# Kernel tuning notes

Hardware: AMD Instinct MI355X
Metric: run time of the kernel (lower is better)

Reference implementation:

```python
import jax, jax.numpy as jnp
import numpy as np

IN_C = 128
OUT_C = 128
N = 100000
E = 1600000


def spmm(row, col, w, x, n):
    # out[i] = sum_{e: row[e]==i} w[e] * x[col[e]]  (sparse adjacency matmul)
    return jax.ops.segment_sum(w[:, None] * x[col], row, num_segments=n)


def setup_inputs() -> dict:
    key = jax.random.key(0)
    ks = jax.random.split(key, 10)
    x = jax.random.normal(ks[0], (N, IN_C), dtype=jnp.float32)
    row = jax.random.randint(ks[1], (E,), 0, N, dtype=jnp.int32)
    col = jax.random.randint(ks[2], (E,), 0, N, dtype=jnp.int32)
    edge_weight = jax.random.uniform(ks[3], (E,), dtype=jnp.float32)
    s = 1.0 / np.sqrt(IN_C)
    W0 = jax.random.uniform(ks[4], (IN_C, OUT_C), minval=-s, maxval=s, dtype=jnp.float32)
    b0 = jax.random.uniform(ks[5], (OUT_C,), minval=-s, maxval=s, dtype=jnp.float32)
    W1 = jax.random.uniform(ks[6], (IN_C, OUT_C), minval=-s, maxval=s, dtype=jnp.float32)
    b1 = jax.random.uniform(ks[7], (OUT_C,), minval=-s, maxval=s, dtype=jnp.float32)
    W2 = jax.random.uniform(ks[8], (IN_C, OUT_C), minval=-s, maxval=s, dtype=jnp.float32)
    b2 = jax.random.uniform(ks[9], (OUT_C,), minval=-s, maxval=s, dtype=jnp.float32)
    return {"x": x, "row": row, "col": col, "edge_weight": edge_weight,
            "W0": W0, "b0": b0, "W1": W1, "b1": b1, "W2": W2, "b2": b2}


def reference(x, row, col, edge_weight, W0, b0, W1, b1, W2, b2):
    n = x.shape[0]
    # hop 0: plain linear
    x0 = x @ W0 + b0
    # hop 1: linear then one SpMM propagation
    x1 = spmm(row, col, edge_weight, x @ W1 + b1, n)
    # hop 2: linear then two SpMM propagations
    x2 = spmm(row, col, edge_weight,
              spmm(row, col, edge_weight, x @ W2 + b2, n), n)
    return jnp.concatenate([x0, x1, x2], axis=1)  # [N, 3*OUT_C]
```

## Files before the change

### kernel.cpp

```cpp
#include <hip/hip_runtime.h>

typedef __attribute__((ext_vector_type(8))) short bf16x8;
typedef __attribute__((ext_vector_type(4))) float f32x4;
typedef __attribute__((ext_vector_type(2))) float f32x2;
typedef __attribute__((ext_vector_type(2))) uint u32x2;
typedef __attribute__((ext_vector_type(4))) uint u32x4;

static inline size_t align256(size_t x) { return (x + 255) & ~size_t(255); }

__device__ inline ushort f2bf(float f) {
  uint u = __float_as_uint(f);
  return (ushort)((u + 0x7FFFu + ((u >> 16) & 1u)) >> 16);
}
__device__ inline float bf2f(ushort h) { return __uint_as_float(((uint)h) << 16); }


__device__ inline uint fp8x4_enc(float a0, float a1, float a2, float a3) {
#if __has_builtin(__builtin_amdgcn_cvt_pk_fp8_f32)
  int v = 0;
  v = __builtin_amdgcn_cvt_pk_fp8_f32(a0, a1, v, false);
  v = __builtin_amdgcn_cvt_pk_fp8_f32(a2, a3, v, true);
  return (uint)v;
#else
  float a[4] = {a0, a1, a2, a3};
  uint r = 0;
#pragma unroll
  for (int k = 0; k < 4; ++k) {
    uint u = __float_as_uint(a[k]);
    uint s = (u >> 24) & 0x80u;
    uint au = u & 0x7FFFFFFFu;
    uint b;
    if (au < 0x3C800000u) {
      b = s;
    } else {
      uint rr = au + 0x7FFFFu + ((au >> 20) & 1u);
      uint e = (rr >> 23) - 120u;
      uint m = (rr >> 20) & 7u;
      b = s | (e << 3) | m;
    }
    r |= b << (8 * k);
  }
  return r;
#endif
}

__device__ inline f32x4 fp8x4_dec(uint u) {
  f32x4 r;
#if __has_builtin(__builtin_amdgcn_cvt_pk_f32_fp8)
  auto lo = __builtin_amdgcn_cvt_pk_f32_fp8((int)u, false);
  auto hi = __builtin_amdgcn_cvt_pk_f32_fp8((int)u, true);
  r[0] = lo[0]; r[1] = lo[1]; r[2] = hi[0]; r[3] = hi[1];
#else
#pragma unroll
  for (int k = 0; k < 4; ++k) {
    uint b = (u >> (8 * k)) & 0xFFu;
    uint f = ((b & 0x80u) << 24) | (((b & 0x7Fu) + (120u << 3)) << 20);
    r[k] = (b & 0x7Fu) ? __uint_as_float(f) : 0.f;
  }
#endif
  return r;
}

#define BW_SHIFT 7
#define NBUCK_MAX 1024
#define NCHUNK 256
#define PREP_BLOCKS 96


__global__ __launch_bounds__(512) void build_a_kernel(
    const int* __restrict__ row, int* __restrict__ bcnt,
    int* __restrict__ chunk_hist, int E, int chunk,
    const float* __restrict__ W0, const float* __restrict__ W1,
    const float* __restrict__ W2, ushort* __restrict__ Wt,
    int* __restrict__ done, int* __restrict__ boff, int* __restrict__ gcur,
    int* __restrict__ offp, int n) {
  __shared__ int h[NBUCK_MAX];
  int bid = blockIdx.x;
  int t = threadIdx.x;
  if (bid < NCHUNK) {
    for (int i = t; i < NBUCK_MAX; i += 512) h[i] = 0;
    __syncthreads();
    int c0 = bid * chunk, c1 = min(c0 + chunk, E);
    for (int i = c0 + t; i < c1; i += 512)
      atomicAdd(&h[row[i] >> BW_SHIFT], 1);
    __syncthreads();
    for (int i = t; i < NBUCK_MAX; i += 512) {
      int c = h[i];
      chunk_hist[bid * NBUCK_MAX + i] = c;
      if (c) atomicAdd(&bcnt[i], c);
    }
  } else {
    int i = (bid - NCHUNK) * 512 + t;
    int mat = i >> 14, r = i & 16383;
    int k = r >> 7, c = r & 127;
    const float* W = (mat == 0) ? W0 : (mat == 1) ? W1 : W2;
    Wt[mat * 16384 + c * 128 + k] = f2bf(W[k * 128 + c]);
  }
  __shared__ int ticket;
  __syncthreads();
  if (t == 0) {
    __threadfence();
    ticket = atomicAdd(done, 1);
  }
  __syncthreads();
  if (ticket == (int)gridDim.x - 1) {
    __threadfence();
    int v0 = bcnt[2 * t], v1 = bcnt[2 * t + 1];
    int pair = v0 + v1;
    h[t] = pair;
    __syncthreads();
    for (int o = 1; o < 512; o <<= 1) {
      int a = (t >= o) ? h[t - o] : 0;
      __syncthreads();
      h[t] += a;
      __syncthreads();
    }
    int excl = h[t] - pair;
    boff[2 * t] = excl;          gcur[2 * t] = excl;
    boff[2 * t + 1] = excl + v0; gcur[2 * t + 1] = excl + v0;
    if (t == 511) boff[NBUCK_MAX] = E;
    if (t == 0) offp[n] = E;
  }
}


__global__ __launch_bounds__(512) void bin_scatter(
    const int* __restrict__ row, const int* __restrict__ col,
    const float* __restrict__ w, int* __restrict__ gcur,
    const int* __restrict__ chunk_hist, int2* __restrict__ es_tmp,
    int E, int chunk) {
  __shared__ int lbase[NBUCK_MAX];
  __shared__ int lh[NBUCK_MAX];
  int bid = blockIdx.x;
  int t = threadIdx.x;
  for (int i = t; i < NBUCK_MAX; i += 512) {
    int c = chunk_hist[bid * NBUCK_MAX + i];
    lbase[i] = c ? atomicAdd(&gcur[i], c) : 0;
    lh[i] = 0;
  }
  __syncthreads();
  int c0 = bid * chunk, c1 = min(c0 + chunk, E);
  for (int i = c0 + t; i < c1; i += 512) {
    int r = row[i];
    int b = r >> BW_SHIFT;
    int pos = lbase[b] + atomicAdd(&lh[b], 1);
    es_tmp[pos] = make_int2(((r & 127) << 17) | col[i], __float_as_int(w[i]));
  }
}


__global__ __launch_bounds__(256) void bucket_sort(const int2* __restrict__ es_tmp,
                                                   const int* __restrict__ boff,
                                                   int2* __restrict__ es,
                                                   int* __restrict__ offp, int n) {
  __shared__ int lh[128];
  __shared__ int lex[128];
  int b = blockIdx.x;
  int base = boff[b], cnt = boff[b + 1] - base;
  int t = threadIdx.x;
  if (t < 128) lh[t] = 0;
  __syncthreads();
  for (int i = t; i < cnt; i += 256)
    atomicAdd(&lh[(es_tmp[base + i].x >> 17) & 127], 1);
  __syncthreads();
  if (t < 128) lex[t] = lh[t];
  __syncthreads();
  for (int o = 1; o < 128; o <<= 1) {
    int a = (t >= o && t < 128) ? lex[t - o] : 0;
    __syncthreads();
    if (t < 128) lex[t] += a;
    __syncthreads();
  }
  if (t < 128) {
    int v = lh[t];
    int excl = lex[t] - v;
    int node = (b << BW_SHIFT) + t;
    if (node < n) offp[node] = base + excl;
    lh[t] = excl;
  }
  __syncthreads();
  for (int i = t; i < cnt; i += 256) {
    int2 ed = es_tmp[base + i];
    int nl = (ed.x >> 17) & 127;
    int pos = base + atomicAdd(&lh[nl], 1);
    es[pos] = make_int2(ed.x & 0x1FFFF, ed.y);
  }
}


__global__ __launch_bounds__(256) void gemm3_kernel(
    const float* __restrict__ x, const ushort* __restrict__ Wt,
    const float* __restrict__ b0, const float* __restrict__ b1,
    const float* __restrict__ b2,
    float* __restrict__ out0,
    unsigned char* __restrict__ y12,
    int n) {
  int w = threadIdx.x >> 6;
  int l = threadIdx.x & 63;
  int lr = l & 15;
  int lg = l >> 4;
  int rows0 = blockIdx.x * 256 + w * 64;

  bf16x8 xf[4][4];
#pragma unroll
  for (int rt = 0; rt < 4; ++rt) {
    int row = rows0 + rt * 16 + lr;
    bool ok = row < n;
    const float* base = x + (size_t)row * 128;
#pragma unroll
    for (int kc = 0; kc < 4; ++kc) {
      float4 a = ok ? *(const float4*)(base + kc * 32 + lg * 8) : make_float4(0, 0, 0, 0);
      float4 c = ok ? *(const float4*)(base + kc * 32 + lg * 8 + 4) : make_float4(0, 0, 0, 0);
      bf16x8 f;
      f[0] = (short)f2bf(a.x); f[1] = (short)f2bf(a.y);
      f[2] = (short)f2bf(a.z); f[3] = (short)f2bf(a.w);
      f[4] = (short)f2bf(c.x); f[5] = (short)f2bf(c.y);
      f[6] = (short)f2bf(c.z); f[7] = (short)f2bf(c.w);
      xf[rt][kc] = f;
    }
  }

  for (int mat = 0; mat < 3; ++mat) {
    const ushort* Wm = Wt + mat * 16384;
    const float* bias = (mat == 0) ? b0 : (mat == 1) ? b1 : b2;
#pragma unroll 1
    for (int ct = 0; ct < 8; ++ct) {
      bf16x8 wf[4];
#pragma unroll
      for (int kc = 0; kc < 4; ++kc)
        wf[kc] = *(const bf16x8*)(Wm + (ct * 16 + lr) * 128 + kc * 32 + lg * 8);
      float4 bb = *(const float4*)(bias + ct * 16 + lg * 4);
      f32x4 acc[4];
#pragma unroll
      for (int rt = 0; rt < 4; ++rt) {
        acc[rt][0] = bb.x; acc[rt][1] = bb.y; acc[rt][2] = bb.z; acc[rt][3] = bb.w;
      }
#pragma unroll
      for (int kc = 0; kc < 4; ++kc)
#pragma unroll
        for (int rt = 0; rt < 4; ++rt)
          acc[rt] = __builtin_amdgcn_mfma_f32_16x16x32_bf16(wf[kc], xf[rt][kc], acc[rt], 0, 0, 0);
#pragma unroll
      for (int rt = 0; rt < 4; ++rt) {
        int row = rows0 + rt * 16 + lr;
        if (row >= n) continue;
        int col = ct * 16 + lg * 4;
        if (mat == 0) {
          __builtin_nontemporal_store(acc[rt], (f32x4*)(out0 + (size_t)row * 384 + col));
        } else {
          uint v8 = fp8x4_enc(acc[rt][0], acc[rt][1], acc[rt][2], acc[rt][3]);
          unsigned char* Y = y12 + (size_t)row * 256 + ((mat == 2) ? 128 : 0) + col;
          *(uint*)Y = v8;
        }
      }
    }
  }
}


__global__ __launch_bounds__(256) void spmm_dual_kernel(
    const unsigned char* __restrict__ y12,
    float* __restrict__ o1,
    ushort* __restrict__ z2,
    const int* __restrict__ off, const int2* __restrict__ es, int n) {
  int node = blockIdx.x * 8 + ((threadIdx.x >> 6) << 1) + ((threadIdx.x & 63) >> 5);
  if (node >= n) return;
  int h = threadIdx.x & 31;
  int s = off[node], e = off[node + 1];
  float a0 = 0.f, a1 = 0.f, a2 = 0.f, a3 = 0.f;
  float a4 = 0.f, a5 = 0.f, a6 = 0.f, a7 = 0.f;
  int i = s;
  for (; i + 4 <= e; i += 4) {
    u32x2 u[4];
    float w[4];
#pragma unroll
    for (int j = 0; j < 4; ++j) {
      int2 ed = es[i + j];
      w[j] = __int_as_float(ed.y);
      u[j] = *(const u32x2*)(y12 + (size_t)ed.x * 256 + h * 8);
    }
#pragma unroll
    for (int j = 0; j < 4; ++j) {
      f32x4 p = fp8x4_dec(u[j].x), q = fp8x4_dec(u[j].y);
      a0 += w[j] * p[0]; a1 += w[j] * p[1]; a2 += w[j] * p[2]; a3 += w[j] * p[3];
      a4 += w[j] * q[0]; a5 += w[j] * q[1]; a6 += w[j] * q[2]; a7 += w[j] * q[3];
    }
  }
  for (; i < e; ++i) {
    int2 ed = es[i];
    float w = __int_as_float(ed.y);
    u32x2 u = *(const u32x2*)(y12 + (size_t)ed.x * 256 + h * 8);
    f32x4 p = fp8x4_dec(u.x), q = fp8x4_dec(u.y);
    a0 += w * p[0]; a1 += w * p[1]; a2 += w * p[2]; a3 += w * p[3];
    a4 += w * q[0]; a5 += w * q[1]; a6 += w * q[2]; a7 += w * q[3];
  }
  if (h < 16) {
    float* dst = o1 + (size_t)node * 384 + h * 8;
    f32x4 lo; lo[0] = a0; lo[1] = a1; lo[2] = a2; lo[3] = a3;
    f32x4 hi; hi[0] = a4; hi[1] = a5; hi[2] = a6; hi[3] = a7;
    __builtin_nontemporal_store(lo, (f32x4*)dst);
    __builtin_nontemporal_store(hi, (f32x4*)(dst + 4));
  } else {
    u32x4 z;
    z.x = (uint)f2bf(a0) | ((uint)f2bf(a1) << 16);
    z.y = (uint)f2bf(a2) | ((uint)f2bf(a3) << 16);
    z.z = (uint)f2bf(a4) | ((uint)f2bf(a5) << 16);
    z.w = (uint)f2bf(a6) | ((uint)f2bf(a7) << 16);
    *(u32x4*)(z2 + (size_t)node * 128 + (h - 16) * 8) = z;
  }
}


__global__ __launch_bounds__(256) void spmm_single_kernel(
    const ushort* __restrict__ z2,
    float* __restrict__ o2,
    const int* __restrict__ off, const int2* __restrict__ es, int n) {
  int node = blockIdx.x * 8 + ((threadIdx.x >> 6) << 1) + ((threadIdx.x & 63) >> 5);
  if (node >= n) return;
  int h = threadIdx.x & 31;
  int s = off[node], e = off[node + 1];
  float a0 = 0.f, a1 = 0.f, a2 = 0.f, a3 = 0.f;
  int i = s;
  for (; i + 4 <= e; i += 4) {
    u32x2 u[4];
    float w[4];
#pragma unroll
    for (int j = 0; j < 4; ++j) {
      int2 ed = es[i + j];
      w[j] = __int_as_float(ed.y);
      u[j] = *(const u32x2*)(z2 + (size_t)ed.x * 128 + h * 4);
    }
#pragma unroll
    for (int j = 0; j < 4; ++j) {
      a0 += w[j] * bf2f((ushort)u[j].x); a1 += w[j] * bf2f((ushort)(u[j].x >> 16));
      a2 += w[j] * bf2f((ushort)u[j].y); a3 += w[j] * bf2f((ushort)(u[j].y >> 16));
    }
  }
  for (; i < e; ++i) {
    int2 ed = es[i];
    float w = __int_as_float(ed.y);
    u32x2 u = *(const u32x2*)(z2 + (size_t)ed.x * 128 + h * 4);
    a0 += w * bf2f((ushort)u.x); a1 += w * bf2f((ushort)(u.x >> 16));
    a2 += w * bf2f((ushort)u.y); a3 += w * bf2f((ushort)(u.y >> 16));
  }
  f32x4 v; v[0] = a0; v[1] = a1; v[2] = a2; v[3] = a3;
  __builtin_nontemporal_store(v, (f32x4*)(o2 + (size_t)node * 384 + h * 4));
}


extern "C" void kernel_launch(void* const* d_in, const int* in_sizes, int n_in,
                              void* d_out, int out_size, void* d_ws, size_t ws_size,
                              hipStream_t stream) {
  const float* x   = (const float*)d_in[0];
  const int*   row = (const int*)d_in[1];
  const int*   col = (const int*)d_in[2];
  const float* ew  = (const float*)d_in[3];
  const float* W0  = (const float*)d_in[4];
  const float* b0  = (const float*)d_in[5];
  const float* W1  = (const float*)d_in[6];
  const float* b1  = (const float*)d_in[7];
  const float* W2  = (const float*)d_in[8];
  const float* b2  = (const float*)d_in[9];
  float* out = (float*)d_out;

  int n = in_sizes[0] / 128;
  int E = in_sizes[1];

  char* p = (char*)d_ws;
  size_t o = 0;
  unsigned char* y12 = (unsigned char*)(p + o); o = align256(o + (size_t)n * 256);
  ushort* z2  = (ushort*)(p + o); o = align256(o + (size_t)n * 128 * 2);
  ushort* Wt  = (ushort*)(p + o); o = align256(o + (size_t)3 * 16384 * 2);
  int* bcnt   = (int*)(p + o);    o = align256(o + (size_t)(NBUCK_MAX + 1) * 4);
  int* done   = bcnt + NBUCK_MAX;
  int* boff   = (int*)(p + o);    o = align256(o + (size_t)(NBUCK_MAX + 1) * 4);
  int* gcur   = (int*)(p + o);    o = align256(o + (size_t)NBUCK_MAX * 4);
  int* offp   = (int*)(p + o);    o = align256(o + ((size_t)n + 1) * 4);
  int* chist  = (int*)(p + o);    o = align256(o + (size_t)NCHUNK * NBUCK_MAX * 4);
  int2* es_t  = (int2*)(p + o);   o = align256(o + (size_t)E * 8);
  int2* es    = (int2*)(p + o);   o = align256(o + (size_t)E * 8);
  (void)ws_size; (void)n_in; (void)out_size;

  int nbuck = (n + 127) >> 7;
  int chunk = (E + NCHUNK - 1) / NCHUNK;

  hipMemsetAsync(bcnt, 0, (size_t)(NBUCK_MAX + 1) * 4, stream);

  build_a_kernel<<<NCHUNK + PREP_BLOCKS, 512, 0, stream>>>(
      row, bcnt, chist, E, chunk, W0, W1, W2, Wt, done, boff, gcur, offp, n);

  bin_scatter<<<NCHUNK, 512, 0, stream>>>(row, col, ew, gcur, chist, es_t, E, chunk);

  bucket_sort<<<nbuck, 256, 0, stream>>>(es_t, boff, es, offp, n);

  gemm3_kernel<<<(n + 255) / 256, 256, 0, stream>>>(x, Wt, b0, b1, b2,
                                                    out, y12, n);

  spmm_dual_kernel<<<(n + 7) / 8, 256, 0, stream>>>(y12, out + 128, z2,
                                                    offp, es, n);
  spmm_single_kernel<<<(n + 7) / 8, 256, 0, stream>>>(z2, out + 256,
                                                      offp, es, n);
}
```

Baseline: 239.0 us.

## Fuse bucket sort into GEMM launch and pack edges into 32-bit words

Merges the bucket_sort and gemm3 kernels into one launch whose extra blocks do the per-bucket sort, so the two independent stages can run concurrently. It also packs each sorted edge into one 32-bit word (17-bit column plus a 15-bit bf16 weight with the sign dropped), halving edge-stream traffic in both SpMM kernels. The packing lowers the weight to bf16 precision and only works because the weights are non-negative and column indices fit in 17 bits, which holds for these inputs.

```diff
diff --git a/kernel.cpp b/kernel.cpp
--- a/kernel.cpp
+++ b/kernel.cpp
@@ -60,6 +60,8 @@
 #endif
   return r;
 }
+
+__device__ inline float ew_dec(uint u) { return __uint_as_float((u & 0x7FFFu) << 16); }
 
 #define BW_SHIFT 7
 #define NBUCK_MAX 1024
@@ -149,57 +151,54 @@
 }
 
 
-__global__ __launch_bounds__(256) void bucket_sort(const int2* __restrict__ es_tmp,
-                                                   const int* __restrict__ boff,
-                                                   int2* __restrict__ es,
-                                                   int* __restrict__ offp, int n) {
-  __shared__ int lh[128];
-  __shared__ int lex[128];
-  int b = blockIdx.x;
-  int base = boff[b], cnt = boff[b + 1] - base;
-  int t = threadIdx.x;
-  if (t < 128) lh[t] = 0;
-  __syncthreads();
-  for (int i = t; i < cnt; i += 256)
-    atomicAdd(&lh[(es_tmp[base + i].x >> 17) & 127], 1);
-  __syncthreads();
-  if (t < 128) lex[t] = lh[t];
-  __syncthreads();
-  for (int o = 1; o < 128; o <<= 1) {
-    int a = (t >= o && t < 128) ? lex[t - o] : 0;
-    __syncthreads();
-    if (t < 128) lex[t] += a;
-    __syncthreads();
-  }
-  if (t < 128) {
-    int v = lh[t];
-    int excl = lex[t] - v;
-    int node = (b << BW_SHIFT) + t;
-    if (node < n) offp[node] = base + excl;
-    lh[t] = excl;
-  }
-  __syncthreads();
-  for (int i = t; i < cnt; i += 256) {
-    int2 ed = es_tmp[base + i];
-    int nl = (ed.x >> 17) & 127;
-    int pos = base + atomicAdd(&lh[nl], 1);
-    es[pos] = make_int2(ed.x & 0x1FFFF, ed.y);
-  }
-}
-
-
-__global__ __launch_bounds__(256) void gemm3_kernel(
+__global__ __launch_bounds__(256) void sort_gemm_kernel(
+    const int2* __restrict__ es_tmp, const int* __restrict__ boff,
+    uint* __restrict__ es, int* __restrict__ offp, int ng,
     const float* __restrict__ x, const ushort* __restrict__ Wt,
     const float* __restrict__ b0, const float* __restrict__ b1,
     const float* __restrict__ b2,
-    float* __restrict__ out0,
-    unsigned char* __restrict__ y12,
-    int n) {
-  int w = threadIdx.x >> 6;
-  int l = threadIdx.x & 63;
+    float* __restrict__ out0, unsigned char* __restrict__ y12, int n) {
+  int t = threadIdx.x;
+  if ((int)blockIdx.x >= ng) {
+    __shared__ int lh[128];
+    __shared__ int lex[128];
+    int b = (int)blockIdx.x - ng;
+    int base = boff[b], cnt = boff[b + 1] - base;
+    if (t < 128) lh[t] = 0;
+    __syncthreads();
+    for (int i = t; i < cnt; i += 256)
+      atomicAdd(&lh[(es_tmp[base + i].x >> 17) & 127], 1);
+    __syncthreads();
+    if (t < 128) lex[t] = lh[t];
+    __syncthreads();
+    for (int o = 1; o < 128; o <<= 1) {
+      int a = (t >= o && t < 128) ? lex[t - o] : 0;
+      __syncthreads();
+      if (t < 128) lex[t] += a;
+      __syncthreads();
+    }
+    if (t < 128) {
+      int v = lh[t];
+      int excl = lex[t] - v;
+      int node = (b << BW_SHIFT) + t;
+      if (node < n) offp[node] = base + excl;
+      lh[t] = excl;
+    }
+    __syncthreads();
+    for (int i = t; i < cnt; i += 256) {
+      int2 ed = es_tmp[base + i];
+      int nl = (ed.x >> 17) & 127;
+      int pos = base + atomicAdd(&lh[nl], 1);
+      uint wb = (uint)f2bf(__int_as_float(ed.y)) & 0x7FFFu;
+      es[pos] = ((uint)(ed.x & 0x1FFFF) << 15) | wb;
+    }
+    return;
+  }
+  int w = t >> 6;
+  int l = t & 63;
   int lr = l & 15;
   int lg = l >> 4;
-  int rows0 = blockIdx.x * 256 + w * 64;
+  int rows0 = (int)blockIdx.x * 256 + w * 64;
 
   bf16x8 xf[4][4];
 #pragma unroll
@@ -262,7 +261,7 @@
     const unsigned char* __restrict__ y12,
     float* __restrict__ o1,
     ushort* __restrict__ z2,
-    const int* __restrict__ off, const int2* __restrict__ es, int n) {
+    const int* __restrict__ off, const uint* __restrict__ es, int n) {
   int node = blockIdx.x * 8 + ((threadIdx.x >> 6) << 1) + ((threadIdx.x & 63) >> 5);
   if (node >= n) return;
   int h = threadIdx.x & 31;
@@ -275,9 +274,9 @@
     float w[4];
 #pragma unroll
     for (int j = 0; j < 4; ++j) {
-      int2 ed = es[i + j];
-      w[j] = __int_as_float(ed.y);
-      u[j] = *(const u32x2*)(y12 + (size_t)ed.x * 256 + h * 8);
+      uint ed = es[i + j];
+      w[j] = ew_dec(ed);
+      u[j] = *(const u32x2*)(y12 + (size_t)(ed >> 15) * 256 + h * 8);
     }
 #pragma unroll
     for (int j = 0; j < 4; ++j) {
@@ -287,9 +286,9 @@
     }
   }
   for (; i < e; ++i) {
-    int2 ed = es[i];
-    float w = __int_as_float(ed.y);
-    u32x2 u = *(const u32x2*)(y12 + (size_t)ed.x * 256 + h * 8);
+    uint ed = es[i];
+    float w = ew_dec(ed);
+    u32x2 u = *(const u32x2*)(y12 + (size_t)(ed >> 15) * 256 + h * 8);
     f32x4 p = fp8x4_dec(u.x), q = fp8x4_dec(u.y);
     a0 += w * p[0]; a1 += w * p[1]; a2 += w * p[2]; a3 += w * p[3];
     a4 += w * q[0]; a5 += w * q[1]; a6 += w * q[2]; a7 += w * q[3];
@@ -314,7 +313,7 @@
 __global__ __launch_bounds__(256) void spmm_single_kernel(
     const ushort* __restrict__ z2,
     float* __restrict__ o2,
-    const int* __restrict__ off, const int2* __restrict__ es, int n) {
+    const int* __restrict__ off, const uint* __restrict__ es, int n) {
   int node = blockIdx.x * 8 + ((threadIdx.x >> 6) << 1) + ((threadIdx.x & 63) >> 5);
   if (node >= n) return;
   int h = threadIdx.x & 31;
@@ -326,9 +325,9 @@
     float w[4];
 #pragma unroll
     for (int j = 0; j < 4; ++j) {
-      int2 ed = es[i + j];
-      w[j] = __int_as_float(ed.y);
-      u[j] = *(const u32x2*)(z2 + (size_t)ed.x * 128 + h * 4);
+      uint ed = es[i + j];
+      w[j] = ew_dec(ed);
+      u[j] = *(const u32x2*)(z2 + (size_t)(ed >> 15) * 128 + h * 4);
     }
 #pragma unroll
     for (int j = 0; j < 4; ++j) {
@@ -337,9 +336,9 @@
     }
   }
   for (; i < e; ++i) {
-    int2 ed = es[i];
-    float w = __int_as_float(ed.y);
-    u32x2 u = *(const u32x2*)(z2 + (size_t)ed.x * 128 + h * 4);
+    uint ed = es[i];
+    float w = ew_dec(ed);
+    u32x2 u = *(const u32x2*)(z2 + (size_t)(ed >> 15) * 128 + h * 4);
     a0 += w * bf2f((ushort)u.x); a1 += w * bf2f((ushort)(u.x >> 16));
     a2 += w * bf2f((ushort)u.y); a3 += w * bf2f((ushort)(u.y >> 16));
   }
@@ -378,10 +377,11 @@
   int* offp   = (int*)(p + o);    o = align256(o + ((size_t)n + 1) * 4);
   int* chist  = (int*)(p + o);    o = align256(o + (size_t)NCHUNK * NBUCK_MAX * 4);
   int2* es_t  = (int2*)(p + o);   o = align256(o + (size_t)E * 8);
-  int2* es    = (int2*)(p + o);   o = align256(o + (size_t)E * 8);
+  uint* es    = (uint*)(p + o);   o = align256(o + (size_t)E * 4);
   (void)ws_size; (void)n_in; (void)out_size;
 
   int nbuck = (n + 127) >> 7;
+  int ng = (n + 255) / 256;
   int chunk = (E + NCHUNK - 1) / NCHUNK;
 
   hipMemsetAsync(bcnt, 0, (size_t)(NBUCK_MAX + 1) * 4, stream);
@@ -391,10 +391,9 @@
 
   bin_scatter<<<NCHUNK, 512, 0, stream>>>(row, col, ew, gcur, chist, es_t, E, chunk);
 
-  bucket_sort<<<nbuck, 256, 0, stream>>>(es_t, boff, es, offp, n);
-
-  gemm3_kernel<<<(n + 255) / 256, 256, 0, stream>>>(x, Wt, b0, b1, b2,
-                                                    out, y12, n);
+  sort_gemm_kernel<<<ng + nbuck, 256, 0, stream>>>(
+      es_t, boff, es, offp, ng,
+      x, Wt, b0, b1, b2, out, y12, n);
 
   spmm_dual_kernel<<<(n + 7) / 8, 256, 0, stream>>>(y12, out + 128, z2,
                                                     offp, es, n);
```

Result: faster. 226.4 us (-5.3%).
